# Optimization experiments

Measured on AMD Instinct MI355X. Metric: run time of the kernel, lower is better.

The kernel has to match this reference:

```python
import jax, jax.numpy as jnp
import numpy as np

B, T, EMB_D, HEAD = 8, 2048, 1024, 128


def setup_inputs() -> dict:
    key = jax.random.key(0)
    ks = jax.random.split(key, 7)
    s = 1.0 / np.sqrt(EMB_D)
    return {
        "inputs": jax.random.normal(ks[0], (B, T, EMB_D), dtype=jnp.float32),
        "Wk": jax.random.uniform(ks[1], (EMB_D, HEAD), jnp.float32, -s, s),
        "bk": jax.random.uniform(ks[2], (HEAD,), jnp.float32, -s, s),
        "Wq": jax.random.uniform(ks[3], (EMB_D, HEAD), jnp.float32, -s, s),
        "bq": jax.random.uniform(ks[4], (HEAD,), jnp.float32, -s, s),
        "Wv": jax.random.uniform(ks[5], (EMB_D, HEAD), jnp.float32, -s, s),
        "bv": jax.random.uniform(ks[6], (HEAD,), jnp.float32, -s, s),
    }


def reference(inputs, Wk, bk, Wq, bq, Wv, bv):
    # inputs: [B, T, C]
    Bq, Tq, _ = inputs.shape
    k = inputs @ Wk + bk  # [B, T, H]
    q = inputs @ Wq + bq
    v = inputs @ Wv + bv
    scale = HEAD ** -0.5
    weights = jnp.einsum("bth,bsh->bts", q, k) * scale  # [B, T, T]
    causal = jnp.tril(jnp.ones((Tq, Tq), dtype=bool))
    weights = jnp.where(causal, weights, -jnp.inf)
    # NOTE: original code applies softmax over dim=1 (the query axis), faithfully reproduced
    weights = jax.nn.softmax(weights, axis=1)
    return jnp.einsum("bts,bsh->bth", weights, v)  # [B, T, H]
```

## Files before the change

kernel.cpp:

```cpp
#include <hip/hip_runtime.h>
#include <hip/hip_bf16.h>

#define T_SEQ 2048
#define NBATCH 8
#define EMB 1024
#define HD 128

typedef _Float16 f16_t;
typedef _Float16 f16x8 __attribute__((ext_vector_type(8)));
typedef _Float16 f16x4 __attribute__((ext_vector_type(4)));
typedef float f32x4 __attribute__((ext_vector_type(4)));


__device__ __forceinline__ void g2l(const f16_t* g, f16_t* l) {
    __builtin_amdgcn_global_load_lds(
        (const __attribute__((address_space(1))) unsigned int*)g,
        (__attribute__((address_space(3))) unsigned int*)l, 16, 0, 0);
}

__global__ __launch_bounds__(256) void prep_w(
    const float* __restrict__ Wk, const float* __restrict__ bk,
    const float* __restrict__ Wq, const float* __restrict__ bq,
    const float* __restrict__ Wv, const float* __restrict__ bv,
    f16_t* __restrict__ w2, float* __restrict__ biasc) {
    int n = blockIdx.x;
    const float scale = 0.08838834764831845f;
    const float* W; const float* bias; float sc; int col;
    if (n < 128)      { W = Wq; bias = bq; sc = scale; col = n; }
    else if (n < 256) { W = Wk; bias = bk; sc = 1.0f;  col = n - 128; }
    else              { W = Wv; bias = bv; sc = 1.0f;  col = n - 256; }
    int t = threadIdx.x;
    if (t < 128) {
        int k0 = t * 8;
        f16x8 v;
        #pragma unroll
        for (int i = 0; i < 8; ++i) v[i] = (f16_t)(W[(size_t)(k0 + i) * HD + col] * sc);
        *(f16x8*)&w2[(size_t)(n >> 4) * 16384 + (size_t)(k0 >> 3) * 128 + (n & 15) * 8] = v;
    }
    if (t == 0) biasc[n] = bias[col] * sc;
}

__global__ __launch_bounds__(256) void qkv_gemm(
    const float* __restrict__ X, const f16_t* __restrict__ w2,
    const float* __restrict__ biasc,
    f16_t* __restrict__ q2, f16_t* __restrict__ k2, f16_t* __restrict__ v2) {
    __shared__ f16_t Xs[64 * 40];

    int bid = blockIdx.x;
    int r8 = bid & 7, g = bid >> 3;
    int band = (g / 3) * 8 + r8;
    int i = g % 3;
    int m0 = band * 64, n0 = i * 128;
    int tid = threadIdx.x;
    int lane = tid & 63, w = tid >> 6;
    int quad = lane >> 4, l15 = lane & 15;
    int msub = (w & 1) * 32, nsub = (w >> 1) * 64;

    int srow = tid >> 2;
    int scol = (tid & 3) * 8;

    f32x4 acc[2][4] = {};

    for (int kc = 0; kc < EMB; kc += 32) {
        __syncthreads();
        {
            const float* src = X + (size_t)(m0 + srow) * EMB + kc + scol;
            float4 f0 = *(const float4*)src;
            float4 f1 = *(const float4*)(src + 4);
            union { f16_t h[8]; uint4 u; } pk;
            pk.h[0] = (f16_t)f0.x; pk.h[1] = (f16_t)f0.y;
            pk.h[2] = (f16_t)f0.z; pk.h[3] = (f16_t)f0.w;
            pk.h[4] = (f16_t)f1.x; pk.h[5] = (f16_t)f1.y;
            pk.h[6] = (f16_t)f1.z; pk.h[7] = (f16_t)f1.w;
            *(uint4*)&Xs[srow * 40 + scol] = pk.u;
        }
        __syncthreads();

        f16x8 afr[2];
        #pragma unroll
        for (int mf = 0; mf < 2; ++mf)
            afr[mf] = *(const f16x8*)&Xs[(msub + mf * 16 + l15) * 40 + quad * 8];
        #pragma unroll
        for (int nf = 0; nf < 4; ++nf) {
            int ntile = (n0 + nsub + nf * 16) >> 4;
            f16x8 bfr = *(const f16x8*)&w2[(size_t)ntile * 16384 + (size_t)((kc >> 3) + quad) * 128 + l15 * 8];
            #pragma unroll
            for (int mf = 0; mf < 2; ++mf)
                acc[mf][nf] = __builtin_amdgcn_mfma_f32_16x16x32_f16(afr[mf], bfr, acc[mf][nf], 0, 0, 0);
        }
    }

    #pragma unroll
    for (int nf = 0; nf < 4; ++nf) {
        int ng = n0 + nsub + nf * 16 + l15;
        float bval = biasc[ng];
        #pragma unroll
        for (int mf = 0; mf < 2; ++mf) {
            int rowg = m0 + msub + mf * 16 + quad * 4;
            f32x4 a = acc[mf][nf];
            if (ng < 256) {
                f16_t* dst = (ng < 128) ? q2 : k2;
                int c = ng & 127;
                #pragma unroll
                for (int r = 0; r < 4; ++r) {
                    int row = rowg + r;
                    dst[(size_t)(row >> 4) * 2048 + (c >> 3) * 128 + (row & 15) * 8 + (c & 7)]
                        = (f16_t)(a[r] + bval);
                }
            } else {
                int h = ng - 256;
                f16x4 hv;
                #pragma unroll
                for (int r = 0; r < 4; ++r) hv[r] = (f16_t)(a[r] + bval);
                *(f16x4*)&v2[(size_t)(rowg >> 3) * 1024 + h * 8 + (rowg & 7)] = hv;
            }
        }
    }
}

__global__ __launch_bounds__(256) void zero_all(float4* __restrict__ out4,
                                                float4* __restrict__ colsum4) {
    int bid = blockIdx.x;
    if (bid < 2048) out4[(size_t)bid * 256 + threadIdx.x] = make_float4(0.f, 0.f, 0.f, 0.f);
    else if (bid - 2048 < 16) colsum4[(size_t)(bid - 2048) * 256 + threadIdx.x] = make_float4(0.f, 0.f, 0.f, 0.f);
}

__global__ __launch_bounds__(256, 4) void col_stats(
    const f16_t* __restrict__ q2, const f16_t* __restrict__ k2,
    float* __restrict__ colsum) {
    __shared__ __align__(16) f16_t Ql[4 * 2048];

    int bid = blockIdx.x;
    int b = bid & 7;
    int item = 143 - (bid >> 3);
    int cg = 0, slab = 0, cum = 0;
    for (int c = 0; c < 32; ++c) {
        int n = (32 - c + 3) >> 2;
        if (item < cum + n) { cg = c; slab = item - cum; break; }
        cum += n;
    }
    int tc0 = cg + slab * 4, tc1 = min(tc0 + 4, 32);

    int tid = threadIdx.x, lane = tid & 63, w = tid >> 6;
    int quad = lane >> 4, l15 = lane & 15;
    int brow = b * 128;
    size_t base = (size_t)b * T_SEQ;

    f16x8 bfrs[4][4];
    #pragma unroll
    for (int st = 0; st < 4; ++st) {
        const f16_t* kt = k2 + (size_t)(brow + cg * 4 + st) * 2048 + l15 * 8;
        #pragma unroll
        for (int kf = 0; kf < 4; ++kf)
            bfrs[st][kf] = *(const f16x8*)(kt + (kf * 4 + quad) * 128);
    }

    float lacc[4] = {0.f, 0.f, 0.f, 0.f};

    for (int tc = tc0; tc < tc1; ++tc) {
        int tb = tc * 64;
        __syncthreads();
        const f16_t* qsrc = q2 + (size_t)(brow + tc * 4) * 2048;
        #pragma unroll
        for (int i = 0; i < 4; ++i)
            g2l(qsrc + i * 2048 + tid * 8, Ql + i * 2048 + tid * 8);
        __syncthreads();

        f16x8 afr[4];
        #pragma unroll
        for (int kf = 0; kf < 4; ++kf)
            afr[kf] = *(const f16x8*)&Ql[w * 2048 + (kf * 4 + quad) * 128 + l15 * 8];
        #pragma unroll
        for (int st = 0; st < 4; ++st) {
            f32x4 s = {};
            #pragma unroll
            for (int kf = 0; kf < 4; ++kf)
                s = __builtin_amdgcn_mfma_f32_16x16x32_f16(afr[kf], bfrs[st][kf], s, 0, 0, 0);
            int scol = cg * 64 + st * 16 + l15;
            #pragma unroll
            for (int r = 0; r < 4; ++r) {
                int t = tb + w * 16 + quad * 4 + r;
                if (t >= scol) lacc[st] += __expf(s[r]);
            }
        }
    }

    #pragma unroll
    for (int st = 0; st < 4; ++st) {
        float v = lacc[st];
        v += __shfl_xor(v, 16, 64);
        v += __shfl_xor(v, 32, 64);
        if (quad == 0) atomicAdd(&colsum[base + cg * 64 + st * 16 + l15], v);
    }
}

__global__ __launch_bounds__(256) void inv_l(
    const float* __restrict__ colsum, float* __restrict__ invl) {
    int i = blockIdx.x * 256 + threadIdx.x;
    invl[i] = 1.0f / colsum[i];
}

__global__ __launch_bounds__(256, 4) void attn_out(
    const f16_t* __restrict__ q2, const f16_t* __restrict__ k2,
    const f16_t* __restrict__ v2, const float* __restrict__ invl,
    float* __restrict__ out) {
    __shared__ __align__(16) f16_t Kl[4 * 2048];
    __shared__ __align__(16) f16_t Vl[8 * 1024];
    __shared__ __align__(16) f16_t Pl[32 * 72];

    int bid = blockIdx.x;
    int b = bid & 7;
    int item = 159 - (bid >> 3);
    int g = 0, slab = 0, cum = 0;
    for (int gg = 0; gg < 64; ++gg) {
        int n = (((gg >> 1) + 1) + 7) >> 3;
        if (item < cum + n) { g = gg; slab = item - cum; break; }
        cum += n;
    }
    int nch = (g >> 1) + 1;
    int c0 = slab * 8, c1 = min(c0 + 8, nch);
    int trow = g * 32;

    int tid = threadIdx.x, lane = tid & 63, w = tid >> 6;
    int quad = lane >> 4, l15 = lane & 15;
    int brow = b * 128;
    size_t base = (size_t)b * T_SEQ;

    f16x8 qfr[2][4];
    #pragma unroll
    for (int tt = 0; tt < 2; ++tt) {
        const f16_t* qt = q2 + (size_t)(brow + 2 * g + tt) * 2048 + l15 * 8;
        #pragma unroll
        for (int kf = 0; kf < 4; ++kf)
            qfr[tt][kf] = *(const f16x8*)(qt + (kf * 4 + quad) * 128);
    }

    f32x4 o[2][2] = {};

    for (int c = c0; c < c1; ++c) {
        int sb = c * 64;
        __syncthreads();
        const f16_t* ksrc = k2 + (size_t)(brow + (sb >> 4)) * 2048;
        const f16_t* vsrc = v2 + (((size_t)base + sb) >> 3) * 1024;
        #pragma unroll
        for (int i = 0; i < 4; ++i) {
            g2l(ksrc + i * 2048 + tid * 8, Kl + i * 2048 + tid * 8);
            g2l(vsrc + i * 2048 + tid * 8, Vl + i * 2048 + tid * 8);
        }
        __syncthreads();

        float iv = invl[base + sb + w * 16 + l15];
        int scol = sb + w * 16 + l15;
        f16x8 bfr[4];
        #pragma unroll
        for (int kf = 0; kf < 4; ++kf)
            bfr[kf] = *(const f16x8*)&Kl[w * 2048 + (kf * 4 + quad) * 128 + l15 * 8];
        #pragma unroll
        for (int tt = 0; tt < 2; ++tt) {
            f32x4 s = {};
            #pragma unroll
            for (int kf = 0; kf < 4; ++kf)
                s = __builtin_amdgcn_mfma_f32_16x16x32_f16(qfr[tt][kf], bfr[kf], s, 0, 0, 0);
            #pragma unroll
            for (int r = 0; r < 4; ++r) {
                int t = trow + tt * 16 + quad * 4 + r;
                float pv = (t >= scol) ? __expf(s[r]) * iv : 0.f;
                Pl[(tt * 16 + quad * 4 + r) * 72 + w * 16 + l15] = (f16_t)pv;
            }
        }
        __syncthreads();

        #pragma unroll
        for (int kf2 = 0; kf2 < 2; ++kf2) {
            f16x8 pa0 = *(const f16x8*)&Pl[(l15) * 72 + kf2 * 32 + quad * 8];
            f16x8 pa1 = *(const f16x8*)&Pl[(16 + l15) * 72 + kf2 * 32 + quad * 8];
            #pragma unroll
            for (int hh = 0; hh < 2; ++hh) {
                f16x8 vfr = *(const f16x8*)&Vl[(kf2 * 4 + quad) * 1024 + (w * 32 + hh * 16 + l15) * 8];
                o[0][hh] = __builtin_amdgcn_mfma_f32_16x16x32_f16(pa0, vfr, o[0][hh], 0, 0, 0);
                o[1][hh] = __builtin_amdgcn_mfma_f32_16x16x32_f16(pa1, vfr, o[1][hh], 0, 0, 0);
            }
        }
    }

    #pragma unroll
    for (int tt = 0; tt < 2; ++tt)
        #pragma unroll
        for (int hh = 0; hh < 2; ++hh)
            #pragma unroll
            for (int r = 0; r < 4; ++r)
                atomicAdd(&out[(base + trow + tt * 16 + quad * 4 + r) * HD + w * 32 + hh * 16 + l15],
                          o[tt][hh][r]);
}

extern "C" void kernel_launch(void* const* d_in, const int* in_sizes, int n_in,
                              void* d_out, int out_size, void* d_ws, size_t ws_size,
                              hipStream_t stream) {
    const float* X  = (const float*)d_in[0];
    const float* Wk = (const float*)d_in[1];
    const float* bk = (const float*)d_in[2];
    const float* Wq = (const float*)d_in[3];
    const float* bq = (const float*)d_in[4];
    const float* Wv = (const float*)d_in[5];
    const float* bv = (const float*)d_in[6];
    float* out = (float*)d_out;

    char* ws = (char*)d_ws;
    const size_t W2_B    = 24 * 16384 * 2;
    const size_t BIAS_B  = 2048;
    const size_t QKV_B   = (size_t)NBATCH * T_SEQ * HD * 2;
    const size_t CS_B    = (size_t)NBATCH * T_SEQ * 4;
    f16_t* w2     = (f16_t*)ws;
    float* biasc  = (float*)(ws + W2_B);
    f16_t* q2     = (f16_t*)(ws + W2_B + BIAS_B);
    f16_t* k2     = (f16_t*)(ws + W2_B + BIAS_B + QKV_B);
    f16_t* v2     = (f16_t*)(ws + W2_B + BIAS_B + 2 * QKV_B);
    float* colsum = (float*)(ws + W2_B + BIAS_B + 3 * QKV_B);
    float* invl   = (float*)(ws + W2_B + BIAS_B + 3 * QKV_B + CS_B);

    prep_w<<<dim3(384), dim3(256), 0, stream>>>(Wk, bk, Wq, bq, Wv, bv, w2, biasc);
    qkv_gemm<<<dim3(768), dim3(256), 0, stream>>>(X, w2, biasc, q2, k2, v2);
    zero_all<<<dim3(2064), dim3(256), 0, stream>>>((float4*)out, (float4*)colsum);
    col_stats<<<dim3(1152), dim3(256), 0, stream>>>(q2, k2, colsum);
    inv_l<<<dim3(64), dim3(256), 0, stream>>>(colsum, invl);
    attn_out<<<dim3(1280), dim3(256), 0, stream>>>(q2, k2, v2, invl, out);
}
```

Measured before the change: 185.1 us.

## Fuse zeroing into weight prep, drop inv_l kernel, prefetch X in QKV GEMM

Merges the output and column-sum zeroing into the weight-prep kernel and removes the separate reciprocal kernel, computing 1/colsum inline in attn_out. This cuts two kernel launches and their gaps. The QKV GEMM now works on K chunks of 64 instead of 32, with register double-buffered prefetch of X so global loads overlap the MFMA work. The trade-off is more registers per thread and a redundant division per chunk in attn_out.

```diff
diff --git a/kernel.cpp b/kernel.cpp
--- a/kernel.cpp
+++ b/kernel.cpp
@@ -18,33 +18,41 @@
         (__attribute__((address_space(3))) unsigned int*)l, 16, 0, 0);
 }
 
-__global__ __launch_bounds__(256) void prep_w(
+__global__ __launch_bounds__(256) void prep(
     const float* __restrict__ Wk, const float* __restrict__ bk,
     const float* __restrict__ Wq, const float* __restrict__ bq,
     const float* __restrict__ Wv, const float* __restrict__ bv,
-    f16_t* __restrict__ w2, float* __restrict__ biasc) {
-    int n = blockIdx.x;
-    const float scale = 0.08838834764831845f;
-    const float* W; const float* bias; float sc; int col;
-    if (n < 128)      { W = Wq; bias = bq; sc = scale; col = n; }
-    else if (n < 256) { W = Wk; bias = bk; sc = 1.0f;  col = n - 128; }
-    else              { W = Wv; bias = bv; sc = 1.0f;  col = n - 256; }
+    f16_t* __restrict__ w2, float* __restrict__ biasc,
+    float4* __restrict__ out4, float4* __restrict__ colsum4) {
+    int bid = blockIdx.x;
     int t = threadIdx.x;
-    if (t < 128) {
-        int k0 = t * 8;
-        f16x8 v;
-        #pragma unroll
-        for (int i = 0; i < 8; ++i) v[i] = (f16_t)(W[(size_t)(k0 + i) * HD + col] * sc);
-        *(f16x8*)&w2[(size_t)(n >> 4) * 16384 + (size_t)(k0 >> 3) * 128 + (n & 15) * 8] = v;
-    }
-    if (t == 0) biasc[n] = bias[col] * sc;
+    if (bid < 384) {
+        int n = bid;
+        const float scale = 0.08838834764831845f;
+        const float* W; const float* bias; float sc; int col;
+        if (n < 128)      { W = Wq; bias = bq; sc = scale; col = n; }
+        else if (n < 256) { W = Wk; bias = bk; sc = 1.0f;  col = n - 128; }
+        else              { W = Wv; bias = bv; sc = 1.0f;  col = n - 256; }
+        if (t < 128) {
+            int k0 = t * 8;
+            f16x8 v;
+            #pragma unroll
+            for (int i = 0; i < 8; ++i) v[i] = (f16_t)(W[(size_t)(k0 + i) * HD + col] * sc);
+            *(f16x8*)&w2[(size_t)(n >> 4) * 16384 + (size_t)(k0 >> 3) * 128 + (n & 15) * 8] = v;
+        }
+        if (t == 0) biasc[n] = bias[col] * sc;
+    } else if (bid < 384 + 2048) {
+        out4[(size_t)(bid - 384) * 256 + t] = make_float4(0.f, 0.f, 0.f, 0.f);
+    } else {
+        colsum4[(size_t)(bid - 2432) * 256 + t] = make_float4(0.f, 0.f, 0.f, 0.f);
+    }
 }
 
 __global__ __launch_bounds__(256) void qkv_gemm(
     const float* __restrict__ X, const f16_t* __restrict__ w2,
     const float* __restrict__ biasc,
     f16_t* __restrict__ q2, f16_t* __restrict__ k2, f16_t* __restrict__ v2) {
-    __shared__ f16_t Xs[64 * 40];
+    __shared__ f16_t Xs[64 * 72];
 
     int bid = blockIdx.x;
     int r8 = bid & 7, g = bid >> 3;
@@ -57,37 +65,64 @@
     int msub = (w & 1) * 32, nsub = (w >> 1) * 64;
 
     int srow = tid >> 2;
-    int scol = (tid & 3) * 8;
+    int scg  = (tid & 3) * 16;
+
+    const float* xrow = X + (size_t)(m0 + srow) * EMB + scg;
 
     f32x4 acc[2][4] = {};
-
-    for (int kc = 0; kc < EMB; kc += 32) {
-        __syncthreads();
-        {
-            const float* src = X + (size_t)(m0 + srow) * EMB + kc + scol;
-            float4 f0 = *(const float4*)src;
-            float4 f1 = *(const float4*)(src + 4);
-            union { f16_t h[8]; uint4 u; } pk;
-            pk.h[0] = (f16_t)f0.x; pk.h[1] = (f16_t)f0.y;
-            pk.h[2] = (f16_t)f0.z; pk.h[3] = (f16_t)f0.w;
-            pk.h[4] = (f16_t)f1.x; pk.h[5] = (f16_t)f1.y;
-            pk.h[6] = (f16_t)f1.z; pk.h[7] = (f16_t)f1.w;
-            *(uint4*)&Xs[srow * 40 + scol] = pk.u;
-        }
-        __syncthreads();
-
-        f16x8 afr[2];
-        #pragma unroll
-        for (int mf = 0; mf < 2; ++mf)
-            afr[mf] = *(const f16x8*)&Xs[(msub + mf * 16 + l15) * 40 + quad * 8];
-        #pragma unroll
-        for (int nf = 0; nf < 4; ++nf) {
-            int ntile = (n0 + nsub + nf * 16) >> 4;
-            f16x8 bfr = *(const f16x8*)&w2[(size_t)ntile * 16384 + (size_t)((kc >> 3) + quad) * 128 + l15 * 8];
-            #pragma unroll
-            for (int mf = 0; mf < 2; ++mf)
-                acc[mf][nf] = __builtin_amdgcn_mfma_f32_16x16x32_f16(afr[mf], bfr, acc[mf][nf], 0, 0, 0);
-        }
+    float4 pfA[4], pfB[4];
+    #pragma unroll
+    for (int u = 0; u < 4; ++u) pfA[u] = *(const float4*)(xrow + u * 4);
+    #pragma unroll
+    for (int u = 0; u < 4; ++u) pfB[u] = *(const float4*)(xrow + 64 + u * 4);
+
+    auto stage = [&](float4 (&pf)[4]) {
+        union { f16_t h[8]; uint4 u4; } p0, p1;
+        p0.h[0] = (f16_t)pf[0].x; p0.h[1] = (f16_t)pf[0].y;
+        p0.h[2] = (f16_t)pf[0].z; p0.h[3] = (f16_t)pf[0].w;
+        p0.h[4] = (f16_t)pf[1].x; p0.h[5] = (f16_t)pf[1].y;
+        p0.h[6] = (f16_t)pf[1].z; p0.h[7] = (f16_t)pf[1].w;
+        p1.h[0] = (f16_t)pf[2].x; p1.h[1] = (f16_t)pf[2].y;
+        p1.h[2] = (f16_t)pf[2].z; p1.h[3] = (f16_t)pf[2].w;
+        p1.h[4] = (f16_t)pf[3].x; p1.h[5] = (f16_t)pf[3].y;
+        p1.h[6] = (f16_t)pf[3].z; p1.h[7] = (f16_t)pf[3].w;
+        *(uint4*)&Xs[srow * 72 + scg] = p0.u4;
+        *(uint4*)&Xs[srow * 72 + scg + 8] = p1.u4;
+    };
+    auto compute = [&](int kc) {
+        #pragma unroll
+        for (int ks = 0; ks < 2; ++ks) {
+            f16x8 afr0 = *(const f16x8*)&Xs[(msub + l15) * 72 + ks * 32 + quad * 8];
+            f16x8 afr1 = *(const f16x8*)&Xs[(msub + 16 + l15) * 72 + ks * 32 + quad * 8];
+            #pragma unroll
+            for (int nf = 0; nf < 4; ++nf) {
+                int ntile = (n0 + nsub + nf * 16) >> 4;
+                f16x8 bfr = *(const f16x8*)&w2[(size_t)ntile * 16384 +
+                    (size_t)((kc >> 3) + ks * 4 + quad) * 128 + l15 * 8];
+                acc[0][nf] = __builtin_amdgcn_mfma_f32_16x16x32_f16(afr0, bfr, acc[0][nf], 0, 0, 0);
+                acc[1][nf] = __builtin_amdgcn_mfma_f32_16x16x32_f16(afr1, bfr, acc[1][nf], 0, 0, 0);
+            }
+        }
+    };
+
+    for (int it = 0; it < 16; it += 2) {
+        __syncthreads();
+        stage(pfA);
+        __syncthreads();
+        if (it + 2 < 16) {
+            #pragma unroll
+            for (int u = 0; u < 4; ++u) pfA[u] = *(const float4*)(xrow + (it + 2) * 64 + u * 4);
+        }
+        compute(it * 64);
+
+        __syncthreads();
+        stage(pfB);
+        __syncthreads();
+        if (it + 3 < 16) {
+            #pragma unroll
+            for (int u = 0; u < 4; ++u) pfB[u] = *(const float4*)(xrow + (it + 3) * 64 + u * 4);
+        }
+        compute((it + 1) * 64);
     }
 
     #pragma unroll
@@ -118,13 +153,6 @@
     }
 }
 
-__global__ __launch_bounds__(256) void zero_all(float4* __restrict__ out4,
-                                                float4* __restrict__ colsum4) {
-    int bid = blockIdx.x;
-    if (bid < 2048) out4[(size_t)bid * 256 + threadIdx.x] = make_float4(0.f, 0.f, 0.f, 0.f);
-    else if (bid - 2048 < 16) colsum4[(size_t)(bid - 2048) * 256 + threadIdx.x] = make_float4(0.f, 0.f, 0.f, 0.f);
-}
-
 __global__ __launch_bounds__(256, 4) void col_stats(
     const f16_t* __restrict__ q2, const f16_t* __restrict__ k2,
     float* __restrict__ colsum) {
@@ -194,15 +222,9 @@
     }
 }
 
-__global__ __launch_bounds__(256) void inv_l(
-    const float* __restrict__ colsum, float* __restrict__ invl) {
-    int i = blockIdx.x * 256 + threadIdx.x;
-    invl[i] = 1.0f / colsum[i];
-}
-
 __global__ __launch_bounds__(256, 4) void attn_out(
     const f16_t* __restrict__ q2, const f16_t* __restrict__ k2,
-    const f16_t* __restrict__ v2, const float* __restrict__ invl,
+    const f16_t* __restrict__ v2, const float* __restrict__ colsum,
     float* __restrict__ out) {
     __shared__ __align__(16) f16_t Kl[4 * 2048];
     __shared__ __align__(16) f16_t Vl[8 * 1024];
@@ -249,7 +271,7 @@
         }
         __syncthreads();
 
-        float iv = invl[base + sb + w * 16 + l15];
+        float iv = 1.0f / colsum[base + sb + w * 16 + l15];
         int scol = sb + w * 16 + l15;
         f16x8 bfr[4];
         #pragma unroll
@@ -309,19 +331,16 @@
     const size_t W2_B    = 24 * 16384 * 2;
     const size_t BIAS_B  = 2048;
     const size_t QKV_B   = (size_t)NBATCH * T_SEQ * HD * 2;
-    const size_t CS_B    = (size_t)NBATCH * T_SEQ * 4;
     f16_t* w2     = (f16_t*)ws;
     float* biasc  = (float*)(ws + W2_B);
     f16_t* q2     = (f16_t*)(ws + W2_B + BIAS_B);
     f16_t* k2     = (f16_t*)(ws + W2_B + BIAS_B + QKV_B);
     f16_t* v2     = (f16_t*)(ws + W2_B + BIAS_B + 2 * QKV_B);
     float* colsum = (float*)(ws + W2_B + BIAS_B + 3 * QKV_B);
-    float* invl   = (float*)(ws + W2_B + BIAS_B + 3 * QKV_B + CS_B);
-
-    prep_w<<<dim3(384), dim3(256), 0, stream>>>(Wk, bk, Wq, bq, Wv, bv, w2, biasc);
+
+    prep<<<dim3(2448), dim3(256), 0, stream>>>(Wk, bk, Wq, bq, Wv, bv, w2, biasc,
+                                               (float4*)out, (float4*)colsum);
     qkv_gemm<<<dim3(768), dim3(256), 0, stream>>>(X, w2, biasc, q2, k2, v2);
-    zero_all<<<dim3(2064), dim3(256), 0, stream>>>((float4*)out, (float4*)colsum);
     col_stats<<<dim3(1152), dim3(256), 0, stream>>>(q2, k2, colsum);
-    inv_l<<<dim3(64), dim3(256), 0, stream>>>(colsum, invl);
-    attn_out<<<dim3(1280), dim3(256), 0, stream>>>(q2, k2, v2, invl, out);
-}
+    attn_out<<<dim3(1280), dim3(256), 0, stream>>>(q2, k2, v2, colsum, out);
+}
```

New measurement: 176.1 us. -4.9%, faster.
